# Kernel tuning notes

Hardware: AMD Instinct MI355X
Metric: run time of the kernel (lower is better)

## Reference

```python
import jax, jax.numpy as jnp
import numpy as np

BS, NUM_R, NUM_P, SL_Q = 32, 10, 36, 20
IMG_FEAT, TOPIC_DIM, LSTM = 2048, 600, 512
CAT = IMG_FEAT + TOPIC_DIM  # 2648


def _w(k, fan_in, shape):
    return jax.random.normal(k, shape, jnp.float32) * (1.0 / np.sqrt(fan_in))


def setup_inputs() -> dict:
    key = jax.random.key(0)
    ks = jax.random.split(key, 12)
    img = jax.random.normal(ks[0], (BS, NUM_P, IMG_FEAT), jnp.float32)
    topic_aggregation = jax.random.normal(ks[1], (BS, NUM_R, SL_Q, TOPIC_DIM), jnp.float32)
    ques_not_pad = jax.random.randint(ks[2], (BS, NUM_R, SL_Q), 0, 2, jnp.int32)
    return {
        "img": img,
        "topic_aggregation": topic_aggregation,
        "ques_not_pad": ques_not_pad,
        # GatedTrans for image: img_feature_size -> lstm_hidden_size
        "Wy_img": _w(ks[3], IMG_FEAT, (IMG_FEAT, LSTM)), "by_img": jnp.zeros((LSTM,), jnp.float32),
        "Wg_img": _w(ks[4], IMG_FEAT, (IMG_FEAT, LSTM)), "bg_img": jnp.zeros((LSTM,), jnp.float32),
        # GatedTrans for topic: 2*word_embedding_size -> lstm_hidden_size
        "Wy_t": _w(ks[5], TOPIC_DIM, (TOPIC_DIM, LSTM)), "by_t": jnp.zeros((LSTM,), jnp.float32),
        "Wg_t": _w(ks[6], TOPIC_DIM, (TOPIC_DIM, LSTM)), "bg_t": jnp.zeros((LSTM,), jnp.float32),
        # MLP: cat -> cat -> img_feat
        "W1": _w(ks[7], CAT, (CAT, CAT)), "b1": jnp.zeros((CAT,), jnp.float32),
        "W2": _w(ks[8], CAT, (CAT, IMG_FEAT)), "b2": jnp.zeros((IMG_FEAT,), jnp.float32),
    }


def _gated(x, Wy, by, Wg, bg):
    # GatedTrans: tanh(Linear) * leaky_relu(Linear); dropout is identity (eval)
    return jnp.tanh(x @ Wy + by) * jax.nn.leaky_relu(x @ Wg + bg, negative_slope=0.01)


def reference(img, topic_aggregation, ques_not_pad,
              Wy_img, by_img, Wg_img, bg_img,
              Wy_t, by_t, Wg_t, bg_t,
              W1, b1, W2, b2):
    bs, num_p, img_feat = img.shape
    _, num_r, sl_q, t_dim = topic_aggregation.shape

    # image GatedTrans is identical across rounds -> compute once, broadcast
    v_feat = _gated(img, Wy_img, by_img, Wg_img, bg_img)            # (bs, num_p, lstm)
    v_feat = jnp.broadcast_to(v_feat[:, None], (bs, num_r, num_p, v_feat.shape[-1]))
    v_feat = v_feat.reshape(bs * num_r, num_p, -1)                  # (B, num_p, lstm)

    topic_feat = _gated(topic_aggregation, Wy_t, by_t, Wg_t, bg_t)
    topic_feat = topic_feat.reshape(bs * num_r, sl_q, -1)           # (B, sl_q, lstm)

    mask = ques_not_pad.reshape(bs * num_r, 1, sl_q).astype(jnp.float32)

    vt_score = jnp.einsum('bpl,bsl->bps', v_feat, topic_feat)       # (B, num_p, sl_q)
    vt_score = vt_score * mask + (mask - 1.0) * 10000.0
    vt_score = jax.nn.softmax(vt_score, axis=-1)

    topic_flat = topic_aggregation.reshape(bs * num_r, sl_q, t_dim)
    # broadcast-multiply+sum in original == bmm over sl_q
    vt_att = jnp.einsum('bps,bst->bpt', vt_score, topic_flat)       # (B, num_p, t_dim)

    img_exp = jnp.broadcast_to(img[:, None], (bs, num_r, num_p, img_feat))
    img_exp = img_exp.reshape(bs * num_r, num_p, img_feat)

    h = jnp.concatenate([img_exp, vt_att], axis=-1)                 # (B, num_p, cat)
    h = jax.nn.relu(h @ W1 + b1)
    h = jax.nn.relu(h @ W2 + b2)
    return h.reshape(bs, num_r, num_p, img_feat)
```

## Files before the change

kernel.cpp:

```cpp
#include <hip/hip_runtime.h>
#include <hip/hip_bf16.h>
#include <cstddef>
#include <cstdint>

#define BS_     32
#define NUM_R_  10
#define NUM_P_  36
#define SL_Q_   20
#define IMG_F_  2048
#define TDIM_   600
#define TDIMP_  640
#define LSTM_   512
#define CAT_    2648
#define CATP_K  2688
#define CATP_R  2688
#define CATP_R8 2816

typedef unsigned short ushort_t;
typedef __attribute__((ext_vector_type(8))) short short8;
typedef __attribute__((ext_vector_type(4))) float f32x4;

__device__ __forceinline__ ushort_t f2bf(float f) {
  union { float f; unsigned int u; } v; v.f = f;
  unsigned int r = v.u + 0x7fff + ((v.u >> 16) & 1);
  return (ushort_t)(r >> 16);
}
__device__ __forceinline__ float bf2f(ushort_t u) {
  union { unsigned int u; float f; } v; v.u = ((unsigned int)u) << 16;
  return v.f;
}

typedef __attribute__((address_space(1))) const unsigned int as1_uint;
typedef __attribute__((address_space(3))) unsigned int as3_uint;
__device__ __forceinline__ void gl_lds16(const ushort_t* g, ushort_t* l) {
  __builtin_amdgcn_global_load_lds((as1_uint*)g, (as3_uint*)l, 16, 0, 0);
}

__device__ __forceinline__ void trans_tile(
    const float* __restrict__ in, ushort_t* __restrict__ out,
    int r0, int R, int C, int Rp, int Cp, int bx, int by)
{
  __shared__ float tile[64][65];
  const int t = threadIdx.x;
  const int lc = t & 63, g = t >> 6;
  const int rbase = by * 64, cbase = bx * 64;
#pragma unroll
  for (int i = 0; i < 16; ++i) {
    int lr = g + 4 * i;
    int rr = rbase + lr, cc = cbase + lc;
    tile[lr][lc] = (rr < R && cc < C) ? in[(size_t)(r0 + rr) * C + cc] : 0.f;
  }
  __syncthreads();
#pragma unroll
  for (int i = 0; i < 16; ++i) {
    int wr2 = g + 4 * i;
    int oc = cbase + wr2, orr = rbase + lc;
    if (oc < Cp && orr < Rp)
      out[(size_t)oc * Rp + orr] = f2bf(tile[lc][wr2]);
  }
}

#define CONV_NB_IMG  2304
#define CONV_NB_TOP  4000
#define CONV_TOTAL   6304
#define TJ1_OFF 0
#define TJ2_OFF 256
#define TJ3_OFF 512
#define TJ4_OFF 592
#define TJ5_OFF 672
#define TJ6_OFF 2016
#define TJ7_OFF 2456
#define TJ_TOTAL 3800
#define PREP_TOTAL (CONV_TOTAL + TJ_TOTAL)

__global__ __launch_bounds__(256) void prep_all_k(
    const float* __restrict__ img, ushort_t* __restrict__ img_bf,
    const float* __restrict__ topic, ushort_t* __restrict__ topic_bf,
    const float* __restrict__ Wy_img, ushort_t* __restrict__ WyT_img,
    const float* __restrict__ Wg_img, ushort_t* __restrict__ WgT_img,
    const float* __restrict__ Wy_t,  ushort_t* __restrict__ WyT_t,
    const float* __restrict__ Wg_t,  ushort_t* __restrict__ WgT_t,
    const float* __restrict__ W1,    ushort_t* __restrict__ W1T_top,
    ushort_t* __restrict__ W1T_bot,
    const float* __restrict__ W2,    ushort_t* __restrict__ W2T)
{
  const int bid0 = blockIdx.x;
  if (bid0 < CONV_NB_IMG) {
    int i = bid0 * 256 + threadIdx.x;
    float4 v = reinterpret_cast<const float4*>(img)[i];
    ushort4 o;
    o.x = f2bf(v.x); o.y = f2bf(v.y); o.z = f2bf(v.z); o.w = f2bf(v.w);
    reinterpret_cast<ushort4*>(img_bf)[i] = o;
    return;
  }
  if (bid0 < CONV_TOTAL) {
    const int npc = TDIMP_ >> 2;
    int i = (bid0 - CONV_NB_IMG) * 256 + threadIdx.x;
    int row = i / npc, c4 = (i - row * npc) << 2;
    ushort4 o = make_ushort4(0, 0, 0, 0);
    if (c4 < TDIM_) {
      float4 v = *reinterpret_cast<const float4*>(&topic[(size_t)row * TDIM_ + c4]);
      o.x = f2bf(v.x); o.y = f2bf(v.y); o.z = f2bf(v.z); o.w = f2bf(v.w);
    }
    *reinterpret_cast<ushort4*>(&topic_bf[(size_t)row * TDIMP_ + c4]) = o;
    return;
  }
  const int bid = bid0 - CONV_TOTAL;
  if (bid < TJ2_OFF) {
    int l = bid - TJ1_OFF;
    trans_tile(Wy_img, WyT_img, 0, 2048, 512, 2048, 512, l % 8, l / 8);
  } else if (bid < TJ3_OFF) {
    int l = bid - TJ2_OFF;
    trans_tile(Wg_img, WgT_img, 0, 2048, 512, 2048, 512, l % 8, l / 8);
  } else if (bid < TJ4_OFF) {
    int l = bid - TJ3_OFF;
    trans_tile(Wy_t, WyT_t, 0, 600, 512, TDIMP_, 512, l % 8, l / 8);
  } else if (bid < TJ5_OFF) {
    int l = bid - TJ4_OFF;
    trans_tile(Wg_t, WgT_t, 0, 600, 512, TDIMP_, 512, l % 8, l / 8);
  } else if (bid < TJ6_OFF) {
    int l = bid - TJ5_OFF;
    trans_tile(W1, W1T_top, 0, 2048, CAT_, 2048, CATP_R, l % 42, l / 42);
  } else if (bid < TJ7_OFF) {
    int l = bid - TJ6_OFF;
    trans_tile(W1, W1T_bot, 2048, 600, CAT_, TDIMP_, CATP_R8, l % 44, l / 44);
  } else {
    int l = bid - TJ7_OFF;
    trans_tile(W2, W2T, 0, CAT_, 2048, CATP_K, 2048, l % 32, l / 32);
  }
}

__device__ __forceinline__ void gated_body(
    ushort_t* __restrict__ smem,
    const ushort_t* __restrict__ A,
    const ushort_t* __restrict__ ByT, const ushort_t* __restrict__ BgT,
    const float* __restrict__ by, const float* __restrict__ bg,
    ushort_t* __restrict__ out, int M, int Kp, int bx, int byi)
{
  ushort_t* Als = smem;
  ushort_t* Bls = smem + 8192;
  const int tid = threadIdx.x;
  const int lane = tid & 63, w = tid >> 6;
  const int wr = w >> 1, wc = w & 1;
  const int m0 = byi * 128, n0 = bx * 64;
  const int N = LSTM_;

  const int srow = lane >> 2;
  const int scol = (lane & 3) * 8;
  const ushort_t* gA0 = A + (size_t)(m0 + w * 32 + srow) * Kp + scol;
  const ushort_t* gA1 = gA0 + (size_t)16 * Kp;
  const ushort_t* gBm = (w >> 1) ? BgT : ByT;
  const ushort_t* gB0 = gBm + (size_t)(n0 + (w & 1) * 32 + srow) * Kp + scol;
  const ushort_t* gB1 = gB0 + (size_t)16 * Kp;
  const int dA0 = (w * 32) * 32, dA1 = (w * 32 + 16) * 32;
  const int dB0 = ((w & 1) * 32) * 32, dB1 = ((w & 1) * 32 + 16) * 32;
  const int bm = w >> 1;

#define STAGE_W(BUF, KOFF) do {                                   \
    gl_lds16(gA0 + (KOFF), Als + (BUF) * 4096 + dA0);             \
    gl_lds16(gA1 + (KOFF), Als + (BUF) * 4096 + dA1);             \
    gl_lds16(gB0 + (KOFF), Bls + (BUF) * 4096 + bm * 2048 + dB0); \
    gl_lds16(gB1 + (KOFF), Bls + (BUF) * 4096 + bm * 2048 + dB1); \
  } while (0)

  f32x4 accy[4][2] = {}, accg[4][2] = {};
  short8 af[4], byf[2], bgf[2];

#define GATED_COMP(BUF) do {                                                  \
    _Pragma("unroll")                                                         \
    for (int i = 0; i < 4; ++i)                                               \
      af[i] = *reinterpret_cast<const short8*>(                               \
          Als + (BUF) * 4096 +                                                \
          (wr * 64 + i * 16 + (lane & 15)) * 32 + (lane >> 4) * 8);           \
    _Pragma("unroll")                                                         \
    for (int j = 0; j < 2; ++j) {                                             \
      int boff = (wc * 32 + j * 16 + (lane & 15)) * 32 + (lane >> 4) * 8;     \
      byf[j] = *reinterpret_cast<const short8*>(Bls + (BUF) * 4096 + boff);   \
      bgf[j] = *reinterpret_cast<const short8*>(Bls + (BUF) * 4096 + 2048 + boff); \
    }                                                                         \
    _Pragma("unroll")                                                         \
    for (int i = 0; i < 4; ++i)                                               \
      _Pragma("unroll")                                                       \
      for (int j = 0; j < 2; ++j) {                                           \
        accy[i][j] = __builtin_amdgcn_mfma_f32_16x16x32_bf16(af[i], byf[j], accy[i][j], 0, 0, 0); \
        accg[i][j] = __builtin_amdgcn_mfma_f32_16x16x32_bf16(af[i], bgf[j], accg[i][j], 0, 0, 0); \
      }                                                                       \
  } while (0)

  STAGE_W(0, 0);
  __syncthreads();
  int kb = 0;
  const int nt2 = Kp >> 6;
  for (int i = 0; i < nt2 - 1; ++i) {
    STAGE_W(1, kb + 32);
    GATED_COMP(0);
    __syncthreads();
    STAGE_W(0, kb + 64);
    GATED_COMP(1);
    __syncthreads();
    kb += 64;
  }
  STAGE_W(1, kb + 32);
  GATED_COMP(0);
  __syncthreads();
  GATED_COMP(1);
#undef STAGE_W
#undef GATED_COMP

  const int crow = (lane >> 4) * 4, ccol = lane & 15;
#pragma unroll
  for (int i = 0; i < 4; ++i)
#pragma unroll
    for (int j = 0; j < 2; ++j)
#pragma unroll
      for (int q = 0; q < 4; ++q) {
        int gm = m0 + wr * 64 + i * 16 + crow + q;
        int gn = n0 + wc * 32 + j * 16 + ccol;
        if (gm >= M || gn >= N) continue;
        float y = tanhf(accy[i][j][q] + by[gn]);
        float g = accg[i][j][q] + bg[gn];
        g = (g > 0.f) ? g : 0.01f * g;
        out[(size_t)gm * N + gn] = f2bf(y * g);
      }
}

__device__ __forceinline__ void gemm128_body(
    ushort_t* __restrict__ smem,
    const ushort_t* __restrict__ A, const ushort_t* __restrict__ BT,
    float* __restrict__ outf, int M, int Kp, int N, int bx, int by)
{
  ushort_t* Als = smem;
  ushort_t* Bls = smem + 8192;
  const int tid = threadIdx.x;
  const int lane = tid & 63, w = tid >> 6;
  const int wr = w >> 1, wc = w & 1;
  const int m0 = by * 128, n0 = bx * 128;

  const int srow = lane >> 2;
  const int scol = (lane & 3) * 8;
  const ushort_t* gA0 = A + (size_t)(m0 + w * 32 + srow) * Kp + scol;
  const ushort_t* gA1 = gA0 + (size_t)16 * Kp;
  const ushort_t* gB0 = BT + (size_t)(n0 + w * 32 + srow) * Kp + scol;
  const ushort_t* gB1 = gB0 + (size_t)16 * Kp;
  const int d0 = (w * 32) * 32, d1 = (w * 32 + 16) * 32;

#define STAGE_G(BUF, KOFF) do {                           \
    gl_lds16(gA0 + (KOFF), Als + (BUF) * 4096 + d0);      \
    gl_lds16(gA1 + (KOFF), Als + (BUF) * 4096 + d1);      \
    gl_lds16(gB0 + (KOFF), Bls + (BUF) * 4096 + d0);      \
    gl_lds16(gB1 + (KOFF), Bls + (BUF) * 4096 + d1);      \
  } while (0)

  f32x4 acc[4][4] = {};
  short8 af[4], bfv[4];

#define GEMM_COMP(BUF) do {                                                   \
    _Pragma("unroll")                                                         \
    for (int i = 0; i < 4; ++i)                                               \
      af[i] = *reinterpret_cast<const short8*>(                               \
          Als + (BUF) * 4096 +                                                \
          (wr * 64 + i * 16 + (lane & 15)) * 32 + (lane >> 4) * 8);           \
    _Pragma("unroll")                                                         \
    for (int j = 0; j < 4; ++j)                                               \
      bfv[j] = *reinterpret_cast<const short8*>(                              \
          Bls + (BUF) * 4096 +                                                \
          (wc * 64 + j * 16 + (lane & 15)) * 32 + (lane >> 4) * 8);           \
    _Pragma("unroll")                                                         \
    for (int i = 0; i < 4; ++i)                                               \
      _Pragma("unroll")                                                       \
      for (int j = 0; j < 4; ++j)                                             \
        acc[i][j] = __builtin_amdgcn_mfma_f32_16x16x32_bf16(af[i], bfv[j], acc[i][j], 0, 0, 0); \
  } while (0)

  STAGE_G(0, 0);
  __syncthreads();
  int kb = 0;
  const int nt2 = Kp >> 6;
  for (int i = 0; i < nt2 - 1; ++i) {
    STAGE_G(1, kb + 32);
    GEMM_COMP(0);
    __syncthreads();
    STAGE_G(0, kb + 64);
    GEMM_COMP(1);
    __syncthreads();
    kb += 64;
  }
  STAGE_G(1, kb + 32);
  GEMM_COMP(0);
  __syncthreads();
  GEMM_COMP(1);
#undef STAGE_G
#undef GEMM_COMP

  const int crow = (lane >> 4) * 4, ccol = lane & 15;
#pragma unroll
  for (int i = 0; i < 4; ++i)
#pragma unroll
    for (int j = 0; j < 4; ++j)
#pragma unroll
      for (int q = 0; q < 4; ++q) {
        int gm = m0 + wr * 64 + i * 16 + crow + q;
        int gn = n0 + wc * 64 + j * 16 + ccol;
        if (gm < M && gn < N) outf[(size_t)gm * N + gn] = acc[i][j][q];
      }
}

#define GB_IMG 72
#define GB_TOP 400
#define HB_NB  189
#define MID_TOTAL (GB_IMG + GB_TOP + HB_NB)

__global__ __launch_bounds__(256) void mid_all_k(
    const ushort_t* __restrict__ img_bf,
    const ushort_t* __restrict__ WyT_img, const ushort_t* __restrict__ WgT_img,
    const float* __restrict__ by_img, const float* __restrict__ bg_img,
    ushort_t* __restrict__ v_feat,
    const ushort_t* __restrict__ topic_bf,
    const ushort_t* __restrict__ WyT_t, const ushort_t* __restrict__ WgT_t,
    const float* __restrict__ by_t, const float* __restrict__ bg_t,
    ushort_t* __restrict__ topic_ft,
    const ushort_t* __restrict__ W1T_top, float* __restrict__ himg)
{
  __shared__ ushort_t smem[16384];
  const int bid = blockIdx.x;
  if (bid < GB_IMG) {
    gated_body(smem, img_bf, WyT_img, WgT_img, by_img, bg_img, v_feat,
               1152, 2048, bid & 7, bid >> 3);
  } else if (bid < GB_IMG + GB_TOP) {
    const int l = bid - GB_IMG;
    gated_body(smem, topic_bf, WyT_t, WgT_t, by_t, bg_t, topic_ft,
               6400, TDIMP_, l & 7, l >> 3);
  } else {
    const int l = bid - GB_IMG - GB_TOP;
    gemm128_body(smem, img_bf, W1T_top, himg, 1152, 2048, CAT_,
                 l % 21, l / 21);
  }
}

template<int MF>
__device__ __forceinline__ void gemm8_body(
    ushort_t* __restrict__ lds8, int bx, int by,
    const ushort_t* __restrict__ A, const ushort_t* __restrict__ BT,
    const float* __restrict__ bias, const float* __restrict__ D,
    float* __restrict__ outf, ushort_t* __restrict__ outb,
    int M, int Kp, int N, int ldOutb, int mode, int base)
{
  const int tid = threadIdx.x;
  const int lane = tid & 63, w = tid >> 6;
  const int wr = w >> 2, wc = w & 3;
  const int m0 = by * (MF * 32), n0 = bx * 256;
  const int r15 = lane & 15, lg = lane >> 4;

  const int pr = lane >> 3, hh = lane & 7;
  const int cc = hh ^ pr;
  const int srow_l = (pr << 1) | (cc >> 2);
  const int scol_l = (cc & 3) << 3;

#define STAGE8(b_, s_, kt_) do {                                             \
    const ushort_t* src_ = ((s_) & 1) ? BT : A;                              \
    const int rowb_ = ((s_) & 1) ? n0 : m0;                                  \
    const int kcol_ = (kt_) * 64 + ((s_) >> 1) * 32 + scol_l;                \
    ushort_t* dst_ = &lds8[(b_) * 32768 + (s_) * 8192];                      \
    _Pragma("unroll")                                                        \
    for (int i_ = 0; i_ < 2; ++i_) {                                         \
      int grow_ = rowb_ + w * 32 + i_ * 16 + srow_l;                         \
      gl_lds16(src_ + (size_t)grow_ * Kp + kcol_,                            \
               &dst_[(w * 32 + i_ * 16) * 32]);                              \
    }                                                                        \
  } while (0)

#define LDS_RD(b_, s_, row_) (*reinterpret_cast<const short8*>(              \
    &lds8[(b_) * 32768 + (s_) * 8192 + ((row_) >> 1) * 64 +                  \
          (((((row_) & 1) << 2) | lg) ^ (((row_) >> 1) & 7)) * 8]))

  f32x4 acc[MF][4] = {};
  short8 aR0[MF], aR1[MF];
  short8 bR0[2], bR1[2];
  const int NT = Kp >> 6;

#define PHASE_WAIT() do {                                   \
    asm volatile("s_waitcnt vmcnt(4)" ::: "memory");        \
    __builtin_amdgcn_s_barrier();                           \
    __builtin_amdgcn_sched_barrier(0);                      \
  } while (0)

#define PRELOAD_A(ar_, b_, ks_) do {                                        \
    _Pragma("unroll")                                                       \
    for (int mf_ = 0; mf_ < MF; ++mf_)                                      \
      ar_[mf_] = LDS_RD(b_, (ks_) * 2, wr * (MF * 16) + mf_ * 16 + r15);    \
  } while (0)

#define PRELOAD_B(br_, b_, ks_, nfb_) do {                                  \
    br_[0] = LDS_RD(b_, (ks_) * 2 + 1, wc * 64 + (nfb_) * 16 + r15);        \
    br_[1] = LDS_RD(b_, (ks_) * 2 + 1, wc * 64 + ((nfb_) + 1) * 16 + r15);  \
  } while (0)

#define MFMA_G(ar_, br_, nfb_) do {                                         \
    __builtin_amdgcn_sched_barrier(0);                                      \
    __builtin_amdgcn_s_setprio(1);                                          \
    _Pragma("unroll")                                                       \
    for (int mf_ = 0; mf_ < MF; ++mf_) {                                    \
      acc[mf_][(nfb_)] = __builtin_amdgcn_mfma_f32_16x16x32_bf16(           \
          ar_[mf_], br_[0], acc[mf_][(nfb_)], 0, 0, 0);                     \
      acc[mf_][(nfb_) + 1] = __builtin_amdgcn_mfma_f32_16x16x32_bf16(       \
          ar_[mf_], br_[1], acc[mf_][(nfb_) + 1], 0, 0, 0);                 \
    }                                                                       \
    __builtin_amdgcn_s_setprio(0);                                          \
    __builtin_amdgcn_sched_barrier(0);                                      \
  } while (0)

  STAGE8(0, 0, 0); STAGE8(0, 1, 0); STAGE8(0, 2, 0); STAGE8(0, 3, 0);
  asm volatile("s_waitcnt vmcnt(0)" ::: "memory");
  __builtin_amdgcn_s_barrier();
  __builtin_amdgcn_sched_barrier(0);
  PRELOAD_A(aR0, 0, 0);
  PRELOAD_B(bR0, 0, 0, 0);

  for (int T = 0; T < NT - 1; ++T) {
    const int b = T & 1, nb = b ^ 1;
    STAGE8(nb, 0, T + 1);
    PHASE_WAIT();
    PRELOAD_B(bR1, b, 0, 2);
    MFMA_G(aR0, bR0, 0);
    STAGE8(nb, 1, T + 1);
    PHASE_WAIT();
    PRELOAD_A(aR1, b, 1);
    PRELOAD_B(bR0, b, 1, 0);
    MFMA_G(aR0, bR1, 2);
    STAGE8(nb, 2, T + 1);
    PHASE_WAIT();
    PRELOAD_B(bR1, b, 1, 2);
    MFMA_G(aR1, bR0, 0);
    STAGE8(nb, 3, T + 1);
    PHASE_WAIT();
    PRELOAD_A(aR0, nb, 0);
    PRELOAD_B(bR0, nb, 0, 0);
    MFMA_G(aR1, bR1, 2);
  }
  {
    asm volatile("s_waitcnt vmcnt(0)" ::: "memory");
    __builtin_amdgcn_s_barrier();
    __builtin_amdgcn_sched_barrier(0);
    const int b = (NT - 1) & 1;
    PRELOAD_B(bR1, b, 0, 2);
    MFMA_G(aR0, bR0, 0);
    PRELOAD_A(aR1, b, 1);
    PRELOAD_B(bR0, b, 1, 0);
    MFMA_G(aR0, bR1, 2);
    PRELOAD_B(bR1, b, 1, 2);
    MFMA_G(aR1, bR0, 0);
    MFMA_G(aR1, bR1, 2);
  }
#undef STAGE8
#undef PHASE_WAIT
#undef PRELOAD_A
#undef PRELOAD_B
#undef MFMA_G
#undef LDS_RD

  const int crow = lg * 4;
#pragma unroll
  for (int mf = 0; mf < MF; ++mf) {
#pragma unroll
    for (int nf = 0; nf < 4; ++nf) {
#pragma unroll
      for (int q = 0; q < 4; ++q) {
        int gm = m0 + wr * (MF * 16) + mf * 16 + crow + q;
        int gn = n0 + wc * 64 + nf * 16 + r15;
        if (gm >= M) continue;
        float v = acc[mf][nf][q];
        if (mode == 1) {
          if (gn < ldOutb) {
            float vv = 0.f;
            if (gn < N) {
              int g = base + gm;
              int drow = (g / 360) * 36 + (g % 36);
              vv = v + D[(size_t)drow * CAT_ + gn] + bias[gn];
              vv = vv > 0.f ? vv : 0.f;
            }
            outb[(size_t)gm * ldOutb + gn] = f2bf(vv);
          }
        } else {
          if (gn < N) {
            float vv = v + bias[gn];
            outf[(size_t)gm * N + gn] = vv > 0.f ? vv : 0.f;
          }
        }
      }
    }
  }
}

#define E_NB 253
__global__ __launch_bounds__(512, 2) void mfma_gemm8_eswz_k(
    const ushort_t* __restrict__ A, const ushort_t* __restrict__ BT,
    const float* __restrict__ bias, const float* __restrict__ D,
    ushort_t* __restrict__ outb, int base)
{
  extern __shared__ ushort_t lds8[];
  const int bid = blockIdx.x;
  const int xcd = bid & 7, j = bid >> 3;
  const int wgid = (xcd < 5 ? xcd * 32 : 160 + (xcd - 5) * 31) + j;
  const int bx = wgid % 11, by = wgid / 11;
  gemm8_body<8>(lds8, bx, by, A, BT, bias, D, nullptr, outb,
                5760, TDIMP_, CAT_, CATP_K, 1, base);
}

__global__ __launch_bounds__(512, 2) void mfma_gemm8_e2_k(
    const ushort_t* __restrict__ vt_att, const ushort_t* __restrict__ BT,
    const float* __restrict__ bias, const float* __restrict__ D,
    ushort_t* __restrict__ h1c0, ushort_t* __restrict__ h1c1)
{
  extern __shared__ ushort_t lds8[];
  const int c = blockIdx.x < E_NB ? 0 : 1;
  const int bid = blockIdx.x - c * E_NB;
  const int xcd = bid & 7, j = bid >> 3;
  const int wgid = (xcd < 5 ? xcd * 32 : 160 + (xcd - 5) * 31) + j;
  const int bx = wgid % 11, by = wgid / 11;
  gemm8_body<8>(lds8, bx, by,
                vt_att + (size_t)c * 5760 * TDIMP_, BT, bias, D,
                nullptr, c ? h1c1 : h1c0,
                5760, TDIMP_, CAT_, CATP_K, 1, c * 5760);
}

#define F192_NB 240
__global__ __launch_bounds__(512, 2) void mfma_gemm8_f192_k(
    const ushort_t* __restrict__ h1, const ushort_t* __restrict__ W2T,
    const float* __restrict__ b2, float* __restrict__ outf)
{
  extern __shared__ ushort_t lds8[];
  const int bid = blockIdx.x;
  const int swz = (bid & 7) * 30 + (bid >> 3);
  const int bx = swz & 7, by = swz >> 3;
  gemm8_body<6>(lds8, bx, by, h1, W2T, b2, nullptr, outf, nullptr,
                5760, CATP_K, 2048, 0, 2, 0);
}

__global__ __launch_bounds__(256) void attn_fuse_k(
    const ushort_t* __restrict__ v_feat,
    const ushort_t* __restrict__ topic_feat,
    const float* __restrict__ topic_raw,
    const int*   __restrict__ qnp,
    ushort_t* __restrict__ vt_att)
{
  const int b  = blockIdx.x;
  const int ib = b / NUM_R_;
  __shared__ float tr[SL_Q_][TDIM_];
  __shared__ float msk[SL_Q_];

  const int tid = threadIdx.x;
  {
    const float4* g = reinterpret_cast<const float4*>(topic_raw + (size_t)b * SL_Q_ * TDIM_);
    float4* s = reinterpret_cast<float4*>(&tr[0][0]);
    for (int i = tid; i < SL_Q_ * TDIM_ / 4; i += 256) s[i] = g[i];
  }
  if (tid < SL_Q_) msk[tid] = (float)qnp[b * SL_Q_ + tid];
  __syncthreads();

  const int wave = tid >> 6, lane = tid & 63;
  const ushort_t* tf_b = topic_feat + (size_t)b * SL_Q_ * LSTM_;

  for (int p = wave; p < NUM_P_; p += 4) {
    const ushort_t* v = v_feat + ((size_t)ib * NUM_P_ + p) * LSTM_;
    float vr[8];
    {
      short8 vv = *reinterpret_cast<const short8*>(&v[lane * 8]);
#pragma unroll
      for (int k = 0; k < 8; ++k) vr[k] = bf2f((ushort_t)vv[k]);
    }

    float sc[SL_Q_];
#pragma unroll
    for (int s = 0; s < SL_Q_; ++s) {
      short8 tv = *reinterpret_cast<const short8*>(&tf_b[(size_t)s * LSTM_ + lane * 8]);
      float acc = 0.f;
#pragma unroll
      for (int k = 0; k < 8; ++k) acc += vr[k] * bf2f((ushort_t)tv[k]);
#pragma unroll
      for (int off = 32; off > 0; off >>= 1) acc += __shfl_xor(acc, off, 64);
      sc[s] = acc;
    }
    float mx = -1e30f;
#pragma unroll
    for (int s = 0; s < SL_Q_; ++s) {
      float m = msk[s];
      sc[s] = sc[s] * m + (m - 1.f) * 10000.f;
      mx = fmaxf(mx, sc[s]);
    }
    float sum = 0.f;
#pragma unroll
    for (int s = 0; s < SL_Q_; ++s) { sc[s] = expf(sc[s] - mx); sum += sc[s]; }
    const float inv = 1.f / sum;

    ushort_t* outp = vt_att + ((size_t)b * NUM_P_ + p) * TDIMP_;
    for (int t = lane; t < TDIMP_; t += 64) {
      float acc = 0.f;
      if (t < TDIM_) {
#pragma unroll
        for (int s = 0; s < SL_Q_; ++s) acc += sc[s] * tr[s][t];
        acc *= inv;
      }
      outp[t] = f2bf(t < TDIM_ ? acc : 0.f);
    }
  }
}

extern "C" void kernel_launch(void* const* d_in, const int* in_sizes, int n_in,
                              void* d_out, int out_size, void* d_ws, size_t ws_size,
                              hipStream_t stream) {
  const float* img    = (const float*)d_in[0];
  const float* topic  = (const float*)d_in[1];
  const int*   qnp    = (const int*)d_in[2];
  const float* Wy_img = (const float*)d_in[3];
  const float* by_img = (const float*)d_in[4];
  const float* Wg_img = (const float*)d_in[5];
  const float* bg_img = (const float*)d_in[6];
  const float* Wy_t   = (const float*)d_in[7];
  const float* by_t   = (const float*)d_in[8];
  const float* Wg_t   = (const float*)d_in[9];
  const float* bg_t   = (const float*)d_in[10];
  const float* W1     = (const float*)d_in[11];
  const float* b1     = (const float*)d_in[12];
  const float* W2     = (const float*)d_in[13];
  const float* b2     = (const float*)d_in[14];
  float* out = (float*)d_out;

  char* base = (char*)d_ws;
  size_t off = 0;
  auto alloc = [&](size_t bytes) {
    void* p = base + off;
    off += (bytes + 255) & ~(size_t)255;
    return p;
  };
  ushort_t* img_bf    = (ushort_t*)alloc((size_t)1152 * 2048 * 2);
  ushort_t* topic_bf  = (ushort_t*)alloc((size_t)6400 * TDIMP_ * 2);
  ushort_t* WyT_img   = (ushort_t*)alloc((size_t)512 * 2048 * 2);
  ushort_t* WgT_img   = (ushort_t*)alloc((size_t)512 * 2048 * 2);
  ushort_t* WyT_t     = (ushort_t*)alloc((size_t)512 * TDIMP_ * 2);
  ushort_t* WgT_t     = (ushort_t*)alloc((size_t)512 * TDIMP_ * 2);
  ushort_t* W1T_top   = (ushort_t*)alloc((size_t)CATP_R * 2048 * 2);
  ushort_t* v_feat    = (ushort_t*)alloc((size_t)1152 * 512 * 2);
  ushort_t* topic_ft  = (ushort_t*)alloc((size_t)6400 * 512 * 2);
  ushort_t* W1T_bot   = (ushort_t*)alloc((size_t)CATP_R8 * TDIMP_ * 2);
  ushort_t* W2T       = (ushort_t*)alloc((size_t)2048 * CATP_K * 2);
  ushort_t* vt_att    = (ushort_t*)alloc((size_t)(11520 + 128) * TDIMP_ * 2);
  float*    himg      = (float*)alloc((size_t)1152 * CAT_ * 4);
  ushort_t* h1c1      = (ushort_t*)alloc((size_t)5888 * CATP_K * 2);
  const bool merged   = (ws_size >= off);
  ushort_t* h1c0      = (ushort_t*)base;

  const dim3 blk(256);

  prep_all_k<<<dim3(PREP_TOTAL), blk, 0, stream>>>(
      img, img_bf, topic, topic_bf,
      Wy_img, WyT_img, Wg_img, WgT_img, Wy_t, WyT_t, Wg_t, WgT_t,
      W1, W1T_top, W1T_bot, W2, W2T);

  mid_all_k<<<dim3(MID_TOTAL), blk, 0, stream>>>(
      img_bf, WyT_img, WgT_img, by_img, bg_img, v_feat,
      topic_bf, WyT_t, WgT_t, by_t, bg_t, topic_ft,
      W1T_top, himg);

  attn_fuse_k<<<dim3(BS_ * NUM_R_), blk, 0, stream>>>(v_feat, topic_ft, topic, qnp, vt_att);

  if (merged) {
    mfma_gemm8_e2_k<<<dim3(2 * E_NB), dim3(512), 131072, stream>>>(
        vt_att, W1T_bot, b1, himg, h1c0, h1c1);
    mfma_gemm8_f192_k<<<dim3(F192_NB), dim3(512), 131072, stream>>>(
        h1c0, W2T, b2, out);
    mfma_gemm8_f192_k<<<dim3(F192_NB), dim3(512), 131072, stream>>>(
        h1c1, W2T, b2, out + (size_t)5760 * IMG_F_);
  } else {
    for (int c = 0; c < 2; ++c) {
      const int mbase = c * 5760;
      mfma_gemm8_eswz_k<<<dim3(E_NB), dim3(512), 131072, stream>>>(
          vt_att + (size_t)mbase * TDIMP_, W1T_bot, b1, himg, h1c0, mbase);
      mfma_gemm8_f192_k<<<dim3(F192_NB), dim3(512), 131072, stream>>>(
          h1c0, W2T, b2, out + (size_t)mbase * IMG_F_);
    }
  }
}
```

Measured before the change: 406.5 us.

## Replace merged W1-bottom GEMM with 128x128 tile double-buffered MFMA kernel

The merged vt_att @ W1_bot GEMM, with the fused residual add of himg, bias and relu, now uses a new 256-thread kernel. Each block computes a 128x128 tile with static double-buffered LDS and direct global-to-LDS loads, giving 1890 blocks instead of 506 large 512-thread blocks that each needed 128KB of dynamic LDS. The goal is better occupancy and load balance across CUs for this short-K (640) GEMM. The cost is less reuse per tile, more global traffic, no XCD-aware block swizzle, and an epilogue that does per-element scalar stores and D loads.

```diff
diff --git a/kernel.cpp b/kernel.cpp
--- a/kernel.cpp
+++ b/kernel.cpp
@@ -335,6 +335,101 @@
     gemm128_body(smem, img_bf, W1T_top, himg, 1152, 2048, CAT_,
                  l % 21, l / 21);
   }
+}
+
+#define E128_PER 945
+__global__ __launch_bounds__(256) void gemm128e_k(
+    const ushort_t* __restrict__ vt, const ushort_t* __restrict__ BT,
+    const float* __restrict__ bias, const float* __restrict__ D,
+    ushort_t* __restrict__ h1c0, ushort_t* __restrict__ h1c1)
+{
+  __shared__ ushort_t Als[2][128 * 32];
+  __shared__ ushort_t Bls[2][128 * 32];
+  const int c = blockIdx.x < E128_PER ? 0 : 1;
+  const int l = blockIdx.x - c * E128_PER;
+  const int bx = l % 21, by = l / 21;
+  const ushort_t* A = vt + (size_t)c * 5760 * TDIMP_;
+  ushort_t* outb = c ? h1c1 : h1c0;
+  const int base = c * 5760;
+  const int Kp = TDIMP_;
+
+  const int tid = threadIdx.x;
+  const int lane = tid & 63, w = tid >> 6;
+  const int wr = w >> 1, wc = w & 1;
+  const int m0 = by * 128, n0 = bx * 128;
+
+  const int srow = lane >> 2;
+  const int scol = (lane & 3) * 8;
+  const ushort_t* gA0 = A + (size_t)(m0 + w * 32 + srow) * Kp + scol;
+  const ushort_t* gA1 = gA0 + (size_t)16 * Kp;
+  const ushort_t* gB0 = BT + (size_t)(n0 + w * 32 + srow) * Kp + scol;
+  const ushort_t* gB1 = gB0 + (size_t)16 * Kp;
+  const int d0 = (w * 32) * 32, d1 = (w * 32 + 16) * 32;
+
+#define STAGE_E(BUF, KOFF) do {                      \
+    gl_lds16(gA0 + (KOFF), &Als[BUF][d0]);           \
+    gl_lds16(gA1 + (KOFF), &Als[BUF][d1]);           \
+    gl_lds16(gB0 + (KOFF), &Bls[BUF][d0]);           \
+    gl_lds16(gB1 + (KOFF), &Bls[BUF][d1]);           \
+  } while (0)
+
+  f32x4 acc[4][4] = {};
+  short8 af[4], bfv[4];
+
+#define COMP_E(BUF) do {                                                      \
+    _Pragma("unroll")                                                         \
+    for (int i = 0; i < 4; ++i)                                               \
+      af[i] = *reinterpret_cast<const short8*>(                               \
+          &Als[BUF][(wr * 64 + i * 16 + (lane & 15)) * 32 + (lane >> 4) * 8]);\
+    _Pragma("unroll")                                                         \
+    for (int j = 0; j < 4; ++j)                                               \
+      bfv[j] = *reinterpret_cast<const short8*>(                              \
+          &Bls[BUF][(wc * 64 + j * 16 + (lane & 15)) * 32 + (lane >> 4) * 8]);\
+    _Pragma("unroll")                                                         \
+    for (int i = 0; i < 4; ++i)                                               \
+      _Pragma("unroll")                                                       \
+      for (int j = 0; j < 4; ++j)                                             \
+        acc[i][j] = __builtin_amdgcn_mfma_f32_16x16x32_bf16(af[i], bfv[j], acc[i][j], 0, 0, 0); \
+  } while (0)
+
+  STAGE_E(0, 0);
+  __syncthreads();
+  int kb = 0;
+  const int nt2 = Kp >> 6;
+  for (int i = 0; i < nt2 - 1; ++i) {
+    STAGE_E(1, kb + 32);
+    COMP_E(0);
+    __syncthreads();
+    STAGE_E(0, kb + 64);
+    COMP_E(1);
+    __syncthreads();
+    kb += 64;
+  }
+  STAGE_E(1, kb + 32);
+  COMP_E(0);
+  __syncthreads();
+  COMP_E(1);
+#undef STAGE_E
+#undef COMP_E
+
+  const int crow = (lane >> 4) * 4, ccol = lane & 15;
+#pragma unroll
+  for (int i = 0; i < 4; ++i)
+#pragma unroll
+    for (int j = 0; j < 4; ++j)
+#pragma unroll
+      for (int q = 0; q < 4; ++q) {
+        int gm = m0 + wr * 64 + i * 16 + crow + q;
+        int gn = n0 + wc * 64 + j * 16 + ccol;
+        float vv = 0.f;
+        if (gn < CAT_) {
+          int g = base + gm;
+          int drow = (g / 360) * 36 + (g % 36);
+          vv = acc[i][j][q] + D[(size_t)drow * CAT_ + gn] + bias[gn];
+          vv = vv > 0.f ? vv : 0.f;
+        }
+        outb[(size_t)gm * CATP_K + gn] = f2bf(vv);
+      }
 }
 
 template<int MF>
@@ -506,23 +601,6 @@
                 5760, TDIMP_, CAT_, CATP_K, 1, base);
 }
 
-__global__ __launch_bounds__(512, 2) void mfma_gemm8_e2_k(
-    const ushort_t* __restrict__ vt_att, const ushort_t* __restrict__ BT,
-    const float* __restrict__ bias, const float* __restrict__ D,
-    ushort_t* __restrict__ h1c0, ushort_t* __restrict__ h1c1)
-{
-  extern __shared__ ushort_t lds8[];
-  const int c = blockIdx.x < E_NB ? 0 : 1;
-  const int bid = blockIdx.x - c * E_NB;
-  const int xcd = bid & 7, j = bid >> 3;
-  const int wgid = (xcd < 5 ? xcd * 32 : 160 + (xcd - 5) * 31) + j;
-  const int bx = wgid % 11, by = wgid / 11;
-  gemm8_body<8>(lds8, bx, by,
-                vt_att + (size_t)c * 5760 * TDIMP_, BT, bias, D,
-                nullptr, c ? h1c1 : h1c0,
-                5760, TDIMP_, CAT_, CATP_K, 1, c * 5760);
-}
-
 #define F192_NB 240
 __global__ __launch_bounds__(512, 2) void mfma_gemm8_f192_k(
     const ushort_t* __restrict__ h1, const ushort_t* __restrict__ W2T,
@@ -664,7 +742,7 @@
   attn_fuse_k<<<dim3(BS_ * NUM_R_), blk, 0, stream>>>(v_feat, topic_ft, topic, qnp, vt_att);
 
   if (merged) {
-    mfma_gemm8_e2_k<<<dim3(2 * E_NB), dim3(512), 131072, stream>>>(
+    gemm128e_k<<<dim3(2 * E128_PER), blk, 0, stream>>>(
         vt_att, W1T_bot, b1, himg, h1c0, h1c1);
     mfma_gemm8_f192_k<<<dim3(F192_NB), dim3(512), 131072, stream>>>(
         h1c0, W2T, b2, out);
```

New measurement: 417.7 us. 1.03x slower.
